# Kernel optimization log

Hardware: AMD Instinct MI355X
Metric: run time of the kernel (lower is better)

## Reference

```python
import jax, jax.numpy as jnp
import numpy as np

DIM = 128
EMB = 8
HID = 128
N = 50000
E = 400000
IN_DIM = 3 * DIM + EMB  # zi, zj, |zi-zj|, type_emb


def setup_inputs() -> dict:
    key = jax.random.key(0)
    ks = jax.random.split(key, 16)
    s = 0.05
    return {
        "z": jax.random.normal(ks[0], (N, DIM), dtype=jnp.float32),
        "edge_index": jax.random.randint(ks[1], (2, E), 0, N, dtype=jnp.int64),
        "edge_type": jax.random.randint(ks[2], (E,), 0, 2, dtype=jnp.int64),
        "type_emb": jax.random.normal(ks[3], (2, EMB), dtype=jnp.float32) * s,
        "ew1": jax.random.normal(ks[4], (IN_DIM, HID), dtype=jnp.float32) * s,
        "eb1": jnp.zeros((HID,), dtype=jnp.float32),
        "ew2": jax.random.normal(ks[5], (HID, 1), dtype=jnp.float32) * s,
        "eb2": jnp.zeros((1,), dtype=jnp.float32),
        "mw1": jax.random.normal(ks[6], (DIM, DIM), dtype=jnp.float32) * s,
        "mb1": jnp.zeros((DIM,), dtype=jnp.float32),
        "mw2": jax.random.normal(ks[7], (DIM, DIM), dtype=jnp.float32) * s,
        "mb2": jnp.zeros((DIM,), dtype=jnp.float32),
        "gamma": jnp.ones((DIM,), dtype=jnp.float32),
        "beta": jnp.zeros((DIM,), dtype=jnp.float32),
    }


def reference(z, edge_index, edge_type, type_emb, ew1, eb1, ew2, eb2,
              mw1, mb1, mw2, mb2, gamma, beta):
    src = edge_index[0]
    dst = edge_index[1]
    n = z.shape[0]

    # --- learn branch: edge MLP -> sigmoid -> segment softmax over src ---
    zi = z[src]              # [E, D]
    zj = z[dst]              # [E, D]
    te = type_emb[edge_type]  # [E, EMB]
    e_in = jnp.concatenate([zi, zj, jnp.abs(zi - zj), te], axis=1)  # [E, 3D+EMB]
    h = jax.nn.relu(e_in @ ew1 + eb1)
    w = jax.nn.sigmoid((h @ ew2 + eb2)[:, 0])  # [E]
    # scatter_reduce amax with include_self on a -1e9-filled buffer
    m = jax.ops.segment_max(w, src, num_segments=n)
    m = jnp.maximum(m, jnp.float32(-1e9))
    w_exp = jnp.exp(w - m[src])
    ssum = jax.ops.segment_sum(w_exp, src, num_segments=n)
    alpha_learned = w_exp / (ssum[src] + 1e-12)

    # --- uniform branch: alpha = 1/deg(src), msg MLP, scatter-add, LayerNorm ---
    deg = jax.ops.segment_sum(jnp.ones((src.shape[0],), z.dtype), src, num_segments=n)
    alpha_u = 1.0 / (deg[src] + 1e-12)
    msg = (jax.nn.relu(zj @ mw1 + mb1) @ mw2 + mb2) * alpha_u[:, None]  # [E, D]
    agg = jax.ops.segment_sum(msg, src, num_segments=n)  # [N, D]
    x = z + agg  # dropout inactive (eval mode)
    mu = jnp.mean(x, axis=-1, keepdims=True)
    var = jnp.mean(jnp.square(x - mu), axis=-1, keepdims=True)
    out = (x - mu) * jax.lax.rsqrt(var + 1e-5) * gamma + beta
    return (out, alpha_learned)
```

## Files before the change

### kernel.cpp

```cpp
#include <hip/hip_runtime.h>
#include <math.h>


typedef short bf16x8 __attribute__((ext_vector_type(8)));
typedef unsigned short ushort8 __attribute__((ext_vector_type(8)));
typedef float f32x4 __attribute__((ext_vector_type(4)));

__device__ inline short bf16_rne(float f) {
    unsigned u = __float_as_uint(f);
    u = (u + 0x7FFFu + ((u >> 16) & 1u)) >> 16;
    return (short)u;
}
__device__ inline float bf16_to_f(unsigned short h) {
    return __uint_as_float(((unsigned)h) << 16);
}

__global__ void prep_all(const float* __restrict__ te, const float* __restrict__ ew1,
                         const float* __restrict__ eb1, const float* __restrict__ mw1,
                         const float* __restrict__ mw2, float* __restrict__ T2,
                         unsigned short* __restrict__ Wap, unsigned short* __restrict__ Wbp,
                         unsigned short* __restrict__ Wcp, unsigned short* __restrict__ Mw1p,
                         unsigned short* __restrict__ Mw2p) {
    int b = blockIdx.x;
    if (b == 0) {
        int t = threadIdx.x;
        int row = t >> 7, j = t & 127;
        float s = eb1[j];
#pragma unroll
        for (int u = 0; u < 8; ++u) s += te[row * 8 + u] * ew1[(384 + u) * 128 + j];
        T2[row * 128 + j] = s;
        return;
    }
    const float* src = (b == 1) ? ew1 : (b == 2) ? ew1 + 128 * 128
                      : (b == 3) ? ew1 + 256 * 128 : (b == 4) ? mw1 : mw2;
    unsigned short* dst = (b == 1) ? Wap : (b == 2) ? Wbp
                         : (b == 3) ? Wcp : (b == 4) ? Mw1p : Mw2p;
    for (int idx = threadIdx.x; idx < 2048; idx += 256) {
        int ks = idx >> 9, ct = (idx >> 6) & 7, l = idx & 63;
        int kbase = ks * 32 + (l >> 4) * 8;
        int col = ct * 16 + (l & 15);
#pragma unroll
        for (int j = 0; j < 8; ++j)
            dst[(size_t)idx * 8 + j] =
                (unsigned short)bf16_rne(src[(size_t)(kbase + j) * 128 + col]);
    }
}

__global__ void deg_count(const int* __restrict__ ei, int* __restrict__ deg, int E) {
    int e = blockIdx.x * 256 + threadIdx.x;
    if (e >= E) return;
    atomicAdd(&deg[ei[e]], 1);
}

__global__ __launch_bounds__(256) void scan_local(const int* __restrict__ deg,
                                                  int* __restrict__ rowstart,
                                                  int* __restrict__ partials, int N) {
    __shared__ int wtot[4];
    int b = blockIdx.x, t = threadIdx.x, lane = t & 63, wid = t >> 6;
    int i0 = b * 1024 + t * 4;
    int v0 = (i0 + 0 < N) ? deg[i0 + 0] : 0;
    int v1 = (i0 + 1 < N) ? deg[i0 + 1] : 0;
    int v2 = (i0 + 2 < N) ? deg[i0 + 2] : 0;
    int v3 = (i0 + 3 < N) ? deg[i0 + 3] : 0;
    int ts = v0 + v1 + v2 + v3;
    int inc = ts;
#pragma unroll
    for (int off = 1; off < 64; off <<= 1) {
        int u = __shfl_up(inc, off);
        if (lane >= off) inc += u;
    }
    if (lane == 63) wtot[wid] = inc;
    __syncthreads();
    int woff = 0;
    if (wid > 0) woff += wtot[0];
    if (wid > 1) woff += wtot[1];
    if (wid > 2) woff += wtot[2];
    int excl = woff + inc - ts;
    if (i0 + 0 < N) rowstart[i0 + 0] = excl;
    if (i0 + 1 < N) rowstart[i0 + 1] = excl + v0;
    if (i0 + 2 < N) rowstart[i0 + 2] = excl + v0 + v1;
    if (i0 + 3 < N) rowstart[i0 + 3] = excl + v0 + v1 + v2;
    if (t == 255) partials[b] = woff + inc;
}

__global__ void scan_partials(int* __restrict__ partials, int nb) {
    int lane = threadIdx.x;
    int v = (lane < nb) ? partials[lane] : 0;
    int inc = v;
#pragma unroll
    for (int off = 1; off < 64; off <<= 1) {
        int u = __shfl_up(inc, off);
        if (lane >= off) inc += u;
    }
    if (lane < nb) partials[lane] = inc - v;
}

__global__ void scan_add(int* __restrict__ rowstart, const int* __restrict__ partials, int N) {
    int i = blockIdx.x * 256 + threadIdx.x;
    if (i < N) rowstart[i] += partials[i >> 10];
}

__global__ void place_edges(const int* __restrict__ ei, const int* __restrict__ etype,
                            int* __restrict__ cursor, const int* __restrict__ rowstart,
                            int4* __restrict__ cinfo, int E) {
    int e = blockIdx.x * 256 + threadIdx.x;
    if (e >= E) return;
    int s = ei[e], d = ei[E + e];
    int slot = rowstart[s] + atomicAdd(&cursor[s], 1);
    cinfo[slot] = make_int4(d, s, etype[e], e);
}

__global__ __launch_bounds__(256) void node_all(
        const float* __restrict__ z, const bf16x8* __restrict__ Ba,
        const bf16x8* __restrict__ Bb, const bf16x8* __restrict__ Bm1,
        const bf16x8* __restrict__ Bm2, const float* __restrict__ mb1,
        const float* __restrict__ mb2, unsigned short* __restrict__ Pa,
        unsigned short* __restrict__ Pb, unsigned short* __restrict__ zb16,
        float* __restrict__ Mx, int M) {
    __shared__ unsigned short Hs[64][136];
    const int l = threadIdx.x & 63;
    const int wv = threadIdx.x >> 6;
    const int c = l & 15, g = l >> 4;
    const int row = blockIdx.x * 64 + wv * 16 + c;
    const int rowc = row < M ? row : M - 1;
    const float* af = z + (size_t)rowc * 128 + g * 8;

    f32x4 acca[8], accb[8], acch[8];
#pragma unroll
    for (int ct = 0; ct < 8; ++ct)
#pragma unroll
        for (int r = 0; r < 4; ++r) { acca[ct][r] = 0.f; accb[ct][r] = 0.f; acch[ct][r] = 0.f; }

    bf16x8 afrag[4];
#pragma unroll
    for (int ks = 0; ks < 4; ++ks) {
        float4 x0 = *(const float4*)(af + ks * 32);
        float4 x1 = *(const float4*)(af + ks * 32 + 4);
        bf16x8 a;
        a[0] = bf16_rne(x0.x); a[1] = bf16_rne(x0.y);
        a[2] = bf16_rne(x0.z); a[3] = bf16_rne(x0.w);
        a[4] = bf16_rne(x1.x); a[5] = bf16_rne(x1.y);
        a[6] = bf16_rne(x1.z); a[7] = bf16_rne(x1.w);
        afrag[ks] = a;
        if (row < M)
            *(ushort8*)(zb16 + (size_t)row * 128 + ks * 32 + g * 8) = (ushort8)a;
    }
#pragma unroll
    for (int ks = 0; ks < 4; ++ks) {
#pragma unroll
        for (int ct = 0; ct < 8; ++ct) {
            acca[ct] = __builtin_amdgcn_mfma_f32_16x16x32_bf16(
                afrag[ks], Ba[(ks * 8 + ct) * 64 + l], acca[ct], 0, 0, 0);
            accb[ct] = __builtin_amdgcn_mfma_f32_16x16x32_bf16(
                afrag[ks], Bb[(ks * 8 + ct) * 64 + l], accb[ct], 0, 0, 0);
            acch[ct] = __builtin_amdgcn_mfma_f32_16x16x32_bf16(
                afrag[ks], Bm1[(ks * 8 + ct) * 64 + l], acch[ct], 0, 0, 0);
        }
    }

#pragma unroll
    for (int r = 0; r < 4; ++r) {
        int rr = blockIdx.x * 64 + wv * 16 + g * 4 + r;
        bool ok = rr < M;
#pragma unroll
        for (int ct = 0; ct < 8; ++ct) {
            int j = ct * 16 + c;
            if (ok) {
                Pa[(size_t)rr * 128 + j] = (unsigned short)bf16_rne(acca[ct][r]);
                Pb[(size_t)rr * 128 + j] = (unsigned short)bf16_rne(accb[ct][r]);
            }
            Hs[wv * 16 + g * 4 + r][j] =
                (unsigned short)bf16_rne(fmaxf(acch[ct][r] + mb1[j], 0.f));
        }
    }
    __syncthreads();

    f32x4 accm[8];
#pragma unroll
    for (int ct = 0; ct < 8; ++ct)
#pragma unroll
        for (int r = 0; r < 4; ++r) accm[ct][r] = 0.f;
#pragma unroll
    for (int ks = 0; ks < 4; ++ks) {
        bf16x8 a = (bf16x8)(*(const ushort8*)&Hs[wv * 16 + c][ks * 32 + g * 8]);
#pragma unroll
        for (int ct = 0; ct < 8; ++ct)
            accm[ct] = __builtin_amdgcn_mfma_f32_16x16x32_bf16(
                a, Bm2[(ks * 8 + ct) * 64 + l], accm[ct], 0, 0, 0);
    }
#pragma unroll
    for (int r = 0; r < 4; ++r) {
        int rr = blockIdx.x * 64 + wv * 16 + g * 4 + r;
        if (rr >= M) continue;
#pragma unroll
        for (int ct = 0; ct < 8; ++ct) {
            int j = ct * 16 + c;
            Mx[(size_t)rr * 128 + j] = accm[ct][r] + mb2[j];
        }
    }
}

__global__ __launch_bounds__(256) void edge_mlp_mfma(
        const unsigned short* __restrict__ zb16, const int4* __restrict__ cinfo,
        const bf16x8* __restrict__ Bfr,
        const float* __restrict__ ew2, const float* __restrict__ eb2,
        const unsigned short* __restrict__ Pa, const unsigned short* __restrict__ Pb,
        const float* __restrict__ T2, float* __restrict__ expw,
        float* __restrict__ ssum, int E) {
    const int l = threadIdx.x & 63;
    const int wv = threadIdx.x >> 6;
    const int c = l & 15, g = l >> 4;
    const int slot0 = blockIdx.x * 64;

    const int ra = slot0 + wv * 16 + c;
    const int4 ciA = cinfo[ra];
    const unsigned short* zi = zb16 + (size_t)ciA.y * 128 + g * 8;
    const unsigned short* zj = zb16 + (size_t)ciA.x * 128 + g * 8;

    f32x4 acc[8];
#pragma unroll
    for (int ct = 0; ct < 8; ++ct)
#pragma unroll
        for (int r = 0; r < 4; ++r) acc[ct][r] = 0.f;

#pragma unroll
    for (int ks = 0; ks < 4; ++ks) {
        ushort8 ui = *(const ushort8*)(zi + ks * 32);
        ushort8 uj = *(const ushort8*)(zj + ks * 32);
        bf16x8 a;
#pragma unroll
        for (int k = 0; k < 8; ++k)
            a[k] = bf16_rne(fabsf(bf16_to_f(ui[k]) - bf16_to_f(uj[k])));
#pragma unroll
        for (int ct = 0; ct < 8; ++ct) {
            bf16x8 b = Bfr[(ks * 8 + ct) * 64 + l];
            acc[ct] = __builtin_amdgcn_mfma_f32_16x16x32_bf16(a, b, acc[ct], 0, 0, 0);
        }
    }

    const int eb = slot0 + wv * 16 + g * 4;
    int4 cr[4];
#pragma unroll
    for (int r = 0; r < 4; ++r) cr[r] = cinfo[eb + r];

    float s[4] = {0.f, 0.f, 0.f, 0.f};
#pragma unroll
    for (int ct = 0; ct < 8; ++ct) {
        int j = ct * 16 + c;
        float w2v = ew2[j];
#pragma unroll
        for (int r = 0; r < 4; ++r) {
            float h = acc[ct][r] + bf16_to_f(Pa[(size_t)cr[r].y * 128 + j])
                                 + bf16_to_f(Pb[(size_t)cr[r].x * 128 + j])
                                 + T2[cr[r].z * 128 + j];
            s[r] = fmaf(fmaxf(h, 0.f), w2v, s[r]);
        }
    }
#pragma unroll
    for (int r = 0; r < 4; ++r) {
        s[r] += __shfl_xor(s[r], 1);
        s[r] += __shfl_xor(s[r], 2);
        s[r] += __shfl_xor(s[r], 4);
        s[r] += __shfl_xor(s[r], 8);
    }
    if (c == 0) {
        const float eb2v = eb2[0];
#pragma unroll
        for (int r = 0; r < 4; ++r) {
            float w = 1.f / (1.f + expf(-(s[r] + eb2v)));
            float ewv = expf(w);
            expw[cr[r].w] = ewv;
            atomicAdd(&ssum[cr[r].y], ewv);
        }
    }
}

__global__ void alpha_k(const float* __restrict__ expw, const int* __restrict__ ei,
                        const float* __restrict__ ssum, float* __restrict__ oa, int E) {
    int e = blockIdx.x * 256 + threadIdx.x;
    if (e >= E) return;
    oa[e] = expw[e] / (ssum[ei[e]] + 1e-12f);
}

__global__ __launch_bounds__(256) void gather_ln(
        const float* __restrict__ z, const float* __restrict__ Mx,
        const int* __restrict__ rowstart, const int* __restrict__ deg,
        const int4* __restrict__ cinfo, const float* __restrict__ gamma,
        const float* __restrict__ beta, float* __restrict__ out, int N) {
    int wid = threadIdx.x >> 6, lane = threadIdx.x & 63;
    int n = blockIdx.x * 4 + wid;
    if (n >= N) return;
    int r0 = rowstart[n], dg = deg[n];
    float2 a0 = make_float2(0.f, 0.f), a1 = make_float2(0.f, 0.f);
    for (int c = 0; c < dg; c += 64) {
        int cnt = min(64, dg - c);
        int myd = (lane < cnt) ? cinfo[r0 + c + lane].x : 0;
        int j = 0;
        for (; j + 1 < cnt; j += 2) {
            int d0 = __shfl(myd, j), d1 = __shfl(myd, j + 1);
            float2 v0 = ((const float2*)(Mx + (size_t)d0 * 128))[lane];
            float2 v1 = ((const float2*)(Mx + (size_t)d1 * 128))[lane];
            a0.x += v0.x; a0.y += v0.y;
            a1.x += v1.x; a1.y += v1.y;
        }
        if (j < cnt) {
            int d0 = __shfl(myd, j);
            float2 v0 = ((const float2*)(Mx + (size_t)d0 * 128))[lane];
            a0.x += v0.x; a0.y += v0.y;
        }
    }
    float inv = 1.f / ((float)dg + 1e-12f);
    size_t base = (size_t)n * 128;
    float2 zz = ((const float2*)(z + base))[lane];
    float x0 = zz.x + (a0.x + a1.x) * inv;
    float x1 = zz.y + (a0.y + a1.y) * inv;
    float s = x0 + x1;
#pragma unroll
    for (int off = 1; off < 64; off <<= 1) s += __shfl_xor(s, off);
    float mu = s * (1.f / 128.f);
    float d0 = x0 - mu, d1 = x1 - mu;
    float v = d0 * d0 + d1 * d1;
#pragma unroll
    for (int off = 1; off < 64; off <<= 1) v += __shfl_xor(v, off);
    float rs = rsqrtf(v * (1.f / 128.f) + 1e-5f);
    float2 gg = ((const float2*)gamma)[lane];
    float2 bb = ((const float2*)beta)[lane];
    float2 o = make_float2(d0 * rs * gg.x + bb.x, d1 * rs * gg.y + bb.y);
    ((float2*)(out + base))[lane] = o;
}

extern "C" void kernel_launch(void* const* d_in, const int* in_sizes, int n_in,
                              void* d_out, int out_size, void* d_ws, size_t ws_size,
                              hipStream_t stream) {
    const float* z     = (const float*)d_in[0];
    const int*   ei    = (const int*)d_in[1];
    const int*   et    = (const int*)d_in[2];
    const float* temb  = (const float*)d_in[3];
    const float* ew1   = (const float*)d_in[4];
    const float* eb1   = (const float*)d_in[5];
    const float* ew2   = (const float*)d_in[6];
    const float* eb2   = (const float*)d_in[7];
    const float* mw1   = (const float*)d_in[8];
    const float* mb1   = (const float*)d_in[9];
    const float* mw2   = (const float*)d_in[10];
    const float* mb2   = (const float*)d_in[11];
    const float* gamma = (const float*)d_in[12];
    const float* beta  = (const float*)d_in[13];

    const int N = in_sizes[0] / 128;
    const int E = in_sizes[2];

    char* ws = (char*)d_ws;
    size_t off = 0;
    auto take = [&](size_t b) { char* p = ws + off; off += (b + 255) & ~(size_t)255; return p; };
    unsigned short* Pa    = (unsigned short*)take((size_t)N * 128 * 2);
    unsigned short* Pb    = (unsigned short*)take((size_t)N * 128 * 2);
    unsigned short* zb16  = (unsigned short*)take((size_t)N * 128 * 2);
    float*          Mx    = (float*)take((size_t)N * 128 * 4);
    char*           z0    = ws + off;
    float*          ssum  = (float*)take((size_t)N * 4);
    int*            deg   = (int*)take((size_t)N * 4);
    int*            cursor= (int*)take((size_t)N * 4);
    size_t          zb    = (size_t)((ws + off) - z0);
    int*            rowst = (int*)take((size_t)N * 4);
    int*            parts = (int*)take(256 * 4);
    int4*           cinfo = (int4*)take((size_t)E * 16);
    float*          expw  = (float*)take((size_t)E * 4);
    float*          T2    = (float*)take(2 * 128 * 4);
    unsigned short* Wap   = (unsigned short*)take(2048 * 8 * 2);
    unsigned short* Wbp   = (unsigned short*)take(2048 * 8 * 2);
    unsigned short* Wcp   = (unsigned short*)take(2048 * 8 * 2);
    unsigned short* Mw1p  = (unsigned short*)take(2048 * 8 * 2);
    unsigned short* Mw2p  = (unsigned short*)take(2048 * 8 * 2);

    float* out_x = (float*)d_out;
    float* out_a = out_x + (size_t)N * 128;

    hipMemsetAsync(z0, 0, zb, stream);
    prep_all<<<6, 256, 0, stream>>>(temb, ew1, eb1, mw1, mw2,
                                    T2, Wap, Wbp, Wcp, Mw1p, Mw2p);

    const int nb = (N + 1023) / 1024;
    deg_count<<<(E + 255) / 256, 256, 0, stream>>>(ei, deg, E);
    scan_local<<<nb, 256, 0, stream>>>(deg, rowst, parts, N);
    scan_partials<<<1, 64, 0, stream>>>(parts, nb);
    scan_add<<<(N + 255) / 256, 256, 0, stream>>>(rowst, parts, N);
    place_edges<<<(E + 255) / 256, 256, 0, stream>>>(ei, et, cursor, rowst, cinfo, E);

    int gb = (N + 63) / 64;
    node_all<<<gb, 256, 0, stream>>>(z, (const bf16x8*)Wap, (const bf16x8*)Wbp,
                                     (const bf16x8*)Mw1p, (const bf16x8*)Mw2p,
                                     mb1, mb2, Pa, Pb, zb16, Mx, N);

    edge_mlp_mfma<<<E / 64, 256, 0, stream>>>(zb16, cinfo, (const bf16x8*)Wcp, ew2, eb2,
                                              Pa, Pb, T2, expw, ssum, E);
    alpha_k<<<(E + 255) / 256, 256, 0, stream>>>(expw, ei, ssum, out_a, E);
    gather_ln<<<(N + 3) / 4, 256, 0, stream>>>(z, Mx, rowst, deg, cinfo, gamma, beta, out_x, N);
}
```

Before: 326.1 us.

## Permute weight columns so MFMA outputs map to contiguous vectorized stores and gathers

```diff
diff --git a/kernel.cpp b/kernel.cpp
--- a/kernel.cpp
+++ b/kernel.cpp
@@ -38,7 +38,7 @@
     for (int idx = threadIdx.x; idx < 2048; idx += 256) {
         int ks = idx >> 9, ct = (idx >> 6) & 7, l = idx & 63;
         int kbase = ks * 32 + (l >> 4) * 8;
-        int col = ct * 16 + (l & 15);
+        int col = (l & 15) * 8 + ct;
 #pragma unroll
         for (int j = 0; j < 8; ++j)
             dst[(size_t)idx * 8 + j] =
@@ -158,20 +158,25 @@
         }
     }
 
+    float4 m10 = *(const float4*)(mb1 + c * 8);
+    float4 m11 = *(const float4*)(mb1 + c * 8 + 4);
+    float m1v[8] = {m10.x, m10.y, m10.z, m10.w, m11.x, m11.y, m11.z, m11.w};
 #pragma unroll
     for (int r = 0; r < 4; ++r) {
         int rr = blockIdx.x * 64 + wv * 16 + g * 4 + r;
         bool ok = rr < M;
+        ushort8 pa8, pb8, h8;
 #pragma unroll
         for (int ct = 0; ct < 8; ++ct) {
-            int j = ct * 16 + c;
-            if (ok) {
-                Pa[(size_t)rr * 128 + j] = (unsigned short)bf16_rne(acca[ct][r]);
-                Pb[(size_t)rr * 128 + j] = (unsigned short)bf16_rne(accb[ct][r]);
-            }
-            Hs[wv * 16 + g * 4 + r][j] =
-                (unsigned short)bf16_rne(fmaxf(acch[ct][r] + mb1[j], 0.f));
-        }
+            pa8[ct] = (unsigned short)bf16_rne(acca[ct][r]);
+            pb8[ct] = (unsigned short)bf16_rne(accb[ct][r]);
+            h8[ct] = (unsigned short)bf16_rne(fmaxf(acch[ct][r] + m1v[ct], 0.f));
+        }
+        if (ok) {
+            *(ushort8*)(Pa + (size_t)rr * 128 + c * 8) = pa8;
+            *(ushort8*)(Pb + (size_t)rr * 128 + c * 8) = pb8;
+        }
+        *(ushort8*)&Hs[wv * 16 + g * 4 + r][c * 8] = h8;
     }
     __syncthreads();
 
@@ -188,15 +193,18 @@
             accm[ct] = __builtin_amdgcn_mfma_f32_16x16x32_bf16(
                 a, Bm2[(ks * 8 + ct) * 64 + l], accm[ct], 0, 0, 0);
     }
+    float4 m20 = *(const float4*)(mb2 + c * 8);
+    float4 m21 = *(const float4*)(mb2 + c * 8 + 4);
 #pragma unroll
     for (int r = 0; r < 4; ++r) {
         int rr = blockIdx.x * 64 + wv * 16 + g * 4 + r;
         if (rr >= M) continue;
-#pragma unroll
-        for (int ct = 0; ct < 8; ++ct) {
-            int j = ct * 16 + c;
-            Mx[(size_t)rr * 128 + j] = accm[ct][r] + mb2[j];
-        }
+        float4 o0 = make_float4(accm[0][r] + m20.x, accm[1][r] + m20.y,
+                                accm[2][r] + m20.z, accm[3][r] + m20.w);
+        float4 o1 = make_float4(accm[4][r] + m21.x, accm[5][r] + m21.y,
+                                accm[6][r] + m21.z, accm[7][r] + m21.w);
+        *(float4*)(Mx + (size_t)rr * 128 + c * 8) = o0;
+        *(float4*)(Mx + (size_t)rr * 128 + c * 8 + 4) = o1;
     }
 }
 
@@ -243,17 +251,23 @@
 #pragma unroll
     for (int r = 0; r < 4; ++r) cr[r] = cinfo[eb + r];
 
+    float4 w20 = *(const float4*)(ew2 + c * 8);
+    float4 w21 = *(const float4*)(ew2 + c * 8 + 4);
+    float w2v[8] = {w20.x, w20.y, w20.z, w20.w, w21.x, w21.y, w21.z, w21.w};
+
     float s[4] = {0.f, 0.f, 0.f, 0.f};
 #pragma unroll
-    for (int ct = 0; ct < 8; ++ct) {
-        int j = ct * 16 + c;
-        float w2v = ew2[j];
-#pragma unroll
-        for (int r = 0; r < 4; ++r) {
-            float h = acc[ct][r] + bf16_to_f(Pa[(size_t)cr[r].y * 128 + j])
-                                 + bf16_to_f(Pb[(size_t)cr[r].x * 128 + j])
-                                 + T2[cr[r].z * 128 + j];
-            s[r] = fmaf(fmaxf(h, 0.f), w2v, s[r]);
+    for (int r = 0; r < 4; ++r) {
+        ushort8 pa8 = *(const ushort8*)(Pa + (size_t)cr[r].y * 128 + c * 8);
+        ushort8 pb8 = *(const ushort8*)(Pb + (size_t)cr[r].x * 128 + c * 8);
+        const float* t2r = T2 + cr[r].z * 128 + c * 8;
+        float4 t20 = *(const float4*)t2r;
+        float4 t21 = *(const float4*)(t2r + 4);
+        float t2v[8] = {t20.x, t20.y, t20.z, t20.w, t21.x, t21.y, t21.z, t21.w};
+#pragma unroll
+        for (int ct = 0; ct < 8; ++ct) {
+            float h = acc[ct][r] + bf16_to_f(pa8[ct]) + bf16_to_f(pb8[ct]) + t2v[ct];
+            s[r] = fmaf(fmaxf(h, 0.f), w2v[ct], s[r]);
         }
     }
 #pragma unroll
```

New measurement: 297.6 us. 8.7% less time.
